# Performance work log

Measured on AMD Instinct MI355X. Metric: run time of the kernel, lower is better.

The kernel has to match this reference:

```python
import jax, jax.numpy as jnp
import numpy as np

N_AGENTS = 8
N_HEADS = 4
HYP = 128   # hypernet_embed
EMB = 32    # mixing_embed_dim


def _hypernet(entities, entity_mask, fc1_w, fc1_b, attn_w, out_w, out_b, fc2_w, fc2_b):
    # entities: [B, ne, ed]; entity_mask: [B, ne] (1 = masked/inactive)
    B, ne, _ = entities.shape
    hd = HYP // N_HEADS
    x1 = jax.nn.relu(entities @ fc1_w + fc1_b)                      # [B, ne, HYP]
    am = entity_mask[:, :N_AGENTS].astype(x1.dtype)                 # [B, na]
    em = entity_mask.astype(x1.dtype)                               # [B, ne]
    # attn_mask[b,i,j] = 1 - (1-am[i])*(1-em[j]): mask if agent i OR entity j inactive
    pre_mask = 1.0 - (1.0 - am)[:, :, None] * (1.0 - em)[:, None, :]  # [B, na, ne]
    # EntityAttentionLayer: agents are the queries, all entities are keys/values
    qkv = x1 @ attn_w                                               # [B, ne, 3*HYP] (no bias)
    q, k, v = jnp.split(qkv, 3, axis=-1)
    q = q[:, :N_AGENTS].reshape(B, N_AGENTS, N_HEADS, hd)
    k = k.reshape(B, ne, N_HEADS, hd)
    v = v.reshape(B, ne, N_HEADS, hd)
    scale = jnp.asarray(np.sqrt(hd), x1.dtype)
    logits = jnp.einsum('bqhd,bkhd->bhqk', q, k) / scale            # [B, H, na, ne]
    m = pre_mask[:, None, :, :]
    # masked softmax; fully-masked rows (torch: -inf -> NaN -> 0) become 0 via *(1-m)
    w = jax.nn.softmax(jnp.where(m > 0, -1e30, logits), axis=-1) * (1.0 - m)
    attn = jnp.einsum('bhqk,bkhd->bqhd', w, v).reshape(B, N_AGENTS, HYP)
    attn = attn @ out_w + out_b                                     # [B, na, HYP]
    keep = (1.0 - am)[:, :, None]                                   # zero masked agents (post_mask)
    attn = attn * keep
    x3 = (attn @ fc2_w + fc2_b) * keep                              # [B, na, EMB]
    return x3


def reference(agent_qs, entities, entity_mask, fc1_w, fc1_b, attn_w, out_w, out_b, fc2_w, fc2_b):
    bs, T, ne, ed = entities.shape
    B = bs * T
    ents = entities.reshape(B, ne, ed)
    emask = entity_mask.reshape(B, ne)
    qs = agent_qs.reshape(B, N_AGENTS)
    # 4 hypernets: 0=hyper_w_1 (matrix), 1=hyper_w_final (vector), 2=hyper_b_1 (vector), 3=V (scalar)
    outs = [_hypernet(ents, emask, fc1_w[i], fc1_b[i], attn_w[i], out_w[i],
                      out_b[i], fc2_w[i], fc2_b[i]) for i in range(4)]
    w1 = jax.nn.softmax(outs[0], axis=-1)                           # [B, na, EMB]
    b1 = outs[2].mean(axis=1)                                       # [B, EMB]
    hidden = jax.nn.elu(jnp.einsum('ba,bae->be', qs, w1) + b1)      # [B, EMB]
    w_final = jax.nn.softmax(outs[1].mean(axis=1), axis=-1)         # [B, EMB]
    v = outs[3].mean(axis=(1, 2))                                   # [B]
    y = jnp.sum(hidden * w_final, axis=-1) + v                      # [B]
    return y.reshape(bs, T, 1)


def setup_inputs() -> dict:
    key = jax.random.key(0)
    ks = jax.random.split(key, 10)
    bs, T, ne, ed = 128, 64, 16, 64
    s = 0.05
    return {
        'agent_qs': jax.random.normal(ks[0], (bs, T, N_AGENTS), jnp.float32),
        'entities': jax.random.normal(ks[1], (bs, T, ne, ed), jnp.float32),
        'entity_mask': jax.random.randint(ks[2], (bs, T, ne), 0, 2, jnp.int32),
        'fc1_w': jax.random.normal(ks[3], (4, ed, HYP), jnp.float32) * s,
        'fc1_b': jax.random.normal(ks[4], (4, HYP), jnp.float32) * s,
        'attn_w': jax.random.normal(ks[5], (4, HYP, 3 * HYP), jnp.float32) * s,
        'out_w': jax.random.normal(ks[6], (4, HYP, HYP), jnp.float32) * s,
        'out_b': jax.random.normal(ks[7], (4, HYP), jnp.float32) * s,
        'fc2_w': jax.random.normal(ks[8], (4, HYP, EMB), jnp.float32) * s,
        'fc2_b': jax.random.normal(ks[9], (4, EMB), jnp.float32) * s,
    }
```

## Files before the change

### kernel.cpp

```cpp
#include <hip/hip_runtime.h>
#include <math.h>

#define NAG 8
#define NE  16
#define ED  64
#define HYPD 128
#define QKVW 384
#define SB 2

#define X1S 132
#define KS  132
#define QS  132

#define OFF_X1    0
#define OFF_SLOG  0
#define OFF_ATTN  4224
#define OFF_K     8448
#define OFF_ATTN2 8448
#define OFF_Q     16896
#define OFF_OUT0  21120
#define OFF_MEANS 22144
#define OFF_EM    22912
#define LDS_BYTES 23040

typedef __attribute__((ext_vector_type(8))) short bf16x8;
typedef __attribute__((ext_vector_type(4))) short bf16x4;
typedef __attribute__((ext_vector_type(4))) float f32x4;

__device__ __forceinline__ short f2bf(float f) {
    union { float f; unsigned u; } c; c.f = f;
    unsigned r = (c.u + 0x7FFFu + ((c.u >> 16) & 1u)) >> 16;
    return (short)r;
}
__device__ __forceinline__ float bf2f(short s) {
    union { unsigned u; float f; } c; c.u = ((unsigned)(unsigned short)s) << 16; return c.f;
}
__device__ __forceinline__ bf16x8 ld_frag(const short* p) {
    bf16x4 lo = *(const bf16x4*)p;
    bf16x4 hi = *(const bf16x4*)(p + 16);
    return __builtin_shufflevector(lo, hi, 0, 1, 2, 3, 4, 5, 6, 7);
}

__global__ void pack_weights(const float* __restrict__ fc1_w,
                             const float* __restrict__ attn_w,
                             const float* __restrict__ out_w,
                             const float* __restrict__ fc2_w,
                             short* __restrict__ ws) {
    int gid = blockIdx.x * 256 + threadIdx.x;
    if (gid >= 608 * 64) return;
    int slot = gid >> 6, l = gid & 63;
    const float* src; int N, nt, kt;
    if (slot < 64) {
        int h = slot >> 4, f = slot & 15;
        nt = f >> 1; kt = f & 1; N = HYPD; src = fc1_w + h * ED * HYPD;
    } else if (slot < 448) {
        int s2 = slot - 64; int h = s2 / 96, f = s2 % 96;
        nt = f >> 2; kt = f & 3; N = QKVW; src = attn_w + h * HYPD * QKVW;
    } else if (slot < 576) {
        int s2 = slot - 448; int h = s2 >> 5, f = s2 & 31;
        nt = f >> 2; kt = f & 3; N = HYPD; src = out_w + h * HYPD * HYPD;
    } else {
        int s2 = slot - 576; int h = s2 >> 3, f = s2 & 7;
        nt = f >> 2; kt = f & 3; N = 32; src = fc2_w + h * HYPD * 32;
    }
    int rg = l >> 4, lc = l & 15;
    bf16x8 fr;
    #pragma unroll
    for (int j = 0; j < 8; ++j) {
        int k = kt * 32 + 4 * rg + (j & 3) + 16 * (j >> 2);
        fr[j] = f2bf(src[k * N + nt * 16 + lc]);
    }
    ((bf16x8*)ws)[slot * 64 + l] = fr;
}

__global__ __launch_bounds__(128, 2) void flexq_mfma(
    const float* __restrict__ agent_qs,
    const float* __restrict__ entities,
    const int*   __restrict__ entity_mask,
    const float* __restrict__ fc1_b,
    const float* __restrict__ out_b,
    const float* __restrict__ fc2_b,
    const short* __restrict__ wfrag,
    float* __restrict__ out, int B)
{
    __shared__ __align__(16) char smem[LDS_BYTES];
    short* x1    = (short*)(smem + OFF_X1);
    float* slog  = (float*)(smem + OFF_SLOG);
    short* attn  = (short*)(smem + OFF_ATTN);
    short* k     = (short*)(smem + OFF_K);
    short* attn2 = (short*)(smem + OFF_ATTN2);
    short* q     = (short*)(smem + OFF_Q);
    short* out0  = (short*)(smem + OFF_OUT0);
    float* means = (float*)(smem + OFF_MEANS);
    float* em    = (float*)(smem + OFF_EM);

    const int tid = threadIdx.x;
    const int l = tid & 63, w = tid >> 6;
    const int rg = l >> 4, lc = l & 15;
    const int b2 = blockIdx.x * SB;
    const bf16x8* WF = (const bf16x8*)wfrag;

    if (tid < 32)
        em[tid] = (entity_mask[(size_t)b2 * NE + tid] != 0) ? 1.0f : 0.0f;

    bf16x8 aent[2][2];
    #pragma unroll
    for (int kt = 0; kt < 2; ++kt)
        #pragma unroll
        for (int mt = 0; mt < 2; ++mt) {
            const float* ap = entities + ((size_t)(b2 + mt) * NE + lc) * ED + kt * 32 + rg * 4;
            float4 lo = *(const float4*)ap;
            float4 hi = *(const float4*)(ap + 16);
            bf16x8 af;
            af[0]=f2bf(lo.x); af[1]=f2bf(lo.y); af[2]=f2bf(lo.z); af[3]=f2bf(lo.w);
            af[4]=f2bf(hi.x); af[5]=f2bf(hi.y); af[6]=f2bf(hi.z); af[7]=f2bf(hi.w);
            aent[kt][mt] = af;
        }
    __syncthreads();

    for (int i = 0; i < 4; ++i) {
        {
            f32x4 acc[2][4];
            #pragma unroll
            for (int mt = 0; mt < 2; ++mt)
                #pragma unroll
                for (int n = 0; n < 4; ++n) acc[mt][n] = (f32x4){0.f,0.f,0.f,0.f};
            #pragma unroll
            for (int kt = 0; kt < 2; ++kt) {
                bf16x8 bn[4];
                #pragma unroll
                for (int n = 0; n < 4; ++n) bn[n] = WF[(i*16 + (4*w+n)*2 + kt)*64 + l];
                #pragma unroll
                for (int mt = 0; mt < 2; ++mt)
                    #pragma unroll
                    for (int n = 0; n < 4; ++n)
                        acc[mt][n] = __builtin_amdgcn_mfma_f32_16x16x32_bf16(aent[kt][mt], bn[n], acc[mt][n], 0,0,0);
            }
            #pragma unroll
            for (int n = 0; n < 4; ++n) {
                float bias = fc1_b[i*HYPD + (4*w+n)*16 + lc];
                #pragma unroll
                for (int mt = 0; mt < 2; ++mt)
                    #pragma unroll
                    for (int r = 0; r < 4; ++r)
                        x1[(16*mt + 4*rg + r)*X1S + (4*w+n)*16 + lc] = f2bf(fmaxf(acc[mt][n][r] + bias, 0.f));
            }
        }
        __syncthreads();

        f32x4 accv[2][4];
        {
            f32x4 acc[2][4];
            #pragma unroll
            for (int mt = 0; mt < 2; ++mt)
                #pragma unroll
                for (int j = 0; j < 4; ++j) acc[mt][j] = (f32x4){0.f,0.f,0.f,0.f};
            #pragma unroll
            for (int kt = 0; kt < 4; ++kt) {
                bf16x8 bj[4];
                #pragma unroll
                for (int j = 0; j < 4; ++j) bj[j] = WF[(64 + i*96 + (w + 2*j)*4 + kt)*64 + l];
                #pragma unroll
                for (int mt = 0; mt < 2; ++mt) {
                    bf16x8 a = ld_frag(x1 + (16*mt + lc)*X1S + kt*32 + rg*4);
                    #pragma unroll
                    for (int j = 0; j < 4; ++j)
                        acc[mt][j] = __builtin_amdgcn_mfma_f32_16x16x32_bf16(a, bj[j], acc[mt][j], 0,0,0);
                }
            }
            if (rg < 2) {
                #pragma unroll
                for (int j = 0; j < 4; ++j)
                    #pragma unroll
                    for (int mt = 0; mt < 2; ++mt)
                        #pragma unroll
                        for (int r = 0; r < 4; ++r)
                            q[(mt*NAG + 4*rg + r)*QS + (w + 2*j)*16 + lc] = f2bf(acc[mt][j][r]);
            }
        }
        {
            f32x4 acc[2][4];
            #pragma unroll
            for (int mt = 0; mt < 2; ++mt)
                #pragma unroll
                for (int j = 0; j < 4; ++j) acc[mt][j] = (f32x4){0.f,0.f,0.f,0.f};
            #pragma unroll
            for (int kt = 0; kt < 4; ++kt) {
                bf16x8 bj[4];
                #pragma unroll
                for (int j = 0; j < 4; ++j) bj[j] = WF[(64 + i*96 + (8 + w + 2*j)*4 + kt)*64 + l];
                #pragma unroll
                for (int mt = 0; mt < 2; ++mt) {
                    bf16x8 a = ld_frag(x1 + (16*mt + lc)*X1S + kt*32 + rg*4);
                    #pragma unroll
                    for (int j = 0; j < 4; ++j)
                        acc[mt][j] = __builtin_amdgcn_mfma_f32_16x16x32_bf16(a, bj[j], acc[mt][j], 0,0,0);
                }
            }
            #pragma unroll
            for (int j = 0; j < 4; ++j)
                #pragma unroll
                for (int mt = 0; mt < 2; ++mt)
                    #pragma unroll
                    for (int r = 0; r < 4; ++r)
                        k[(16*mt + 4*rg + r)*KS + (w + 2*j)*16 + lc] = f2bf(acc[mt][j][r]);
        }
        {
            #pragma unroll
            for (int mt = 0; mt < 2; ++mt)
                #pragma unroll
                for (int j = 0; j < 4; ++j) accv[mt][j] = (f32x4){0.f,0.f,0.f,0.f};
            #pragma unroll
            for (int kt = 0; kt < 4; ++kt) {
                bf16x8 bj[4];
                #pragma unroll
                for (int j = 0; j < 4; ++j) bj[j] = WF[(64 + i*96 + (16 + w + 2*j)*4 + kt)*64 + l];
                #pragma unroll
                for (int mt = 0; mt < 2; ++mt) {
                    bf16x8 a = ld_frag(x1 + (16*mt + lc)*X1S + kt*32 + rg*4);
                    #pragma unroll
                    for (int j = 0; j < 4; ++j)
                        accv[mt][j] = __builtin_amdgcn_mfma_f32_16x16x32_bf16(a, bj[j], accv[mt][j], 0,0,0);
                }
            }
        }
        __syncthreads();

        {
            #pragma unroll
            for (int h = 0; h < 4; ++h) {
                bf16x8 a  = ld_frag(q + (w*NAG + (lc & 7))*QS + h*32 + rg*4);
                bf16x8 bb = ld_frag(k + (w*NE  + lc)*KS       + h*32 + rg*4);
                f32x4 acc = (f32x4){0.f,0.f,0.f,0.f};
                acc = __builtin_amdgcn_mfma_f32_16x16x32_bf16(a, bb, acc, 0,0,0);
                if (rg < 2) {
                    #pragma unroll
                    for (int r = 0; r < 4; ++r)
                        slog[((w*4 + h)*NAG + 4*rg + r)*16 + lc] = acc[r] * 0.17677669529663687f;
                }
            }
        }
        __syncthreads();

        if (tid < 64) {
            int s = tid >> 5, h = (tid >> 3) & 3, qi = tid & 7;
            float am = em[s*NE + qi];
            float* rowp = slog + ((s*4 + h)*NAG + qi)*16;
            float mx = -3.0e38f; bool any = false;
            #pragma unroll
            for (int kk = 0; kk < NE; ++kk)
                if (em[s*NE + kk] == 0.f) { any = true; mx = fmaxf(mx, rowp[kk]); }
            if (am != 0.f || !any) {
                #pragma unroll
                for (int kk = 0; kk < NE; ++kk) rowp[kk] = 0.f;
            } else {
                float eb[NE]; float sum = 0.f;
                #pragma unroll
                for (int kk = 0; kk < NE; ++kk) {
                    float e = (em[s*NE + kk] == 0.f) ? __expf(rowp[kk] - mx) : 0.f;
                    eb[kk] = e; sum += e;
                }
                float inv = 1.f / sum;
                #pragma unroll
                for (int kk = 0; kk < NE; ++kk) rowp[kk] = eb[kk] * inv;
            }
        }
        __syncthreads();

        {
            #pragma unroll
            for (int vt = 0; vt < 4; ++vt) {
                int c = w + 2*vt;
                int h = c >> 1;
                #pragma unroll
                for (int mt = 0; mt < 2; ++mt) {
                    f32x4 pw = *(const f32x4*)(slog + ((mt*4 + h)*NAG + (lc & 7))*16 + 4*rg);
                    bf16x8 a;
                    a[0]=f2bf(pw[0]); a[1]=f2bf(pw[1]); a[2]=f2bf(pw[2]); a[3]=f2bf(pw[3]);
                    a[4]=0; a[5]=0; a[6]=0; a[7]=0;
                    bf16x8 bb;
                    bb[0]=f2bf(accv[mt][vt][0]); bb[1]=f2bf(accv[mt][vt][1]);
                    bb[2]=f2bf(accv[mt][vt][2]); bb[3]=f2bf(accv[mt][vt][3]);
                    bb[4]=0; bb[5]=0; bb[6]=0; bb[7]=0;
                    f32x4 po = (f32x4){0.f,0.f,0.f,0.f};
                    po = __builtin_amdgcn_mfma_f32_16x16x32_bf16(a, bb, po, 0,0,0);
                    if (rg < 2) {
                        #pragma unroll
                        for (int r = 0; r < 4; ++r)
                            attn[(mt*NAG + 4*rg + r)*X1S + c*16 + lc] = f2bf(po[r]);
                    }
                }
            }
        }
        __syncthreads();

        {
            f32x4 acc[4];
            #pragma unroll
            for (int n = 0; n < 4; ++n) acc[n] = (f32x4){0.f,0.f,0.f,0.f};
            #pragma unroll
            for (int kt = 0; kt < 4; ++kt) {
                bf16x8 bn[4];
                #pragma unroll
                for (int n = 0; n < 4; ++n) bn[n] = WF[(448 + i*32 + (4*w+n)*4 + kt)*64 + l];
                bf16x8 a = ld_frag(attn + lc*X1S + kt*32 + rg*4);
                #pragma unroll
                for (int n = 0; n < 4; ++n)
                    acc[n] = __builtin_amdgcn_mfma_f32_16x16x32_bf16(a, bn[n], acc[n], 0,0,0);
            }
            #pragma unroll
            for (int n = 0; n < 4; ++n) {
                float bias = out_b[i*HYPD + (4*w+n)*16 + lc];
                #pragma unroll
                for (int r = 0; r < 4; ++r) {
                    int row = 4*rg + r;
                    float keep = 1.f - em[(row >> 3)*NE + (row & 7)];
                    attn2[row*X1S + (4*w+n)*16 + lc] = f2bf((acc[n][r] + bias) * keep);
                }
            }
        }
        __syncthreads();

        {
            f32x4 acc = (f32x4){0.f,0.f,0.f,0.f};
            #pragma unroll
            for (int kt = 0; kt < 4; ++kt) {
                bf16x8 a = ld_frag(attn2 + lc*X1S + kt*32 + rg*4);
                bf16x8 bfr = WF[(576 + i*8 + w*4 + kt)*64 + l];
                acc = __builtin_amdgcn_mfma_f32_16x16x32_bf16(a, bfr, acc, 0,0,0);
            }
            float bias = fc2_b[i*32 + w*16 + lc];
            float vals[4];
            #pragma unroll
            for (int r = 0; r < 4; ++r) {
                int row = 4*rg + r;
                float keep = 1.f - em[(row >> 3)*NE + (row & 7)];
                vals[r] = (acc[r] + bias) * keep;
            }
            if (i == 0) {
                #pragma unroll
                for (int r = 0; r < 4; ++r)
                    out0[(4*rg + r)*32 + w*16 + lc] = f2bf(vals[r]);
            } else {
                float ps = vals[0] + vals[1] + vals[2] + vals[3];
                ps += __shfl_xor(ps, 16);
                if ((rg & 1) == 0) {
                    int s = rg >> 1;
                    means[(i-1)*64 + s*32 + w*16 + lc] = ps;
                }
            }
        }
        __syncthreads();
    }

    if (l < 32) {
        int s = w, c = l;
        float s1 = means[0*64 + s*32 + c] * 0.125f;
        float b1 = means[1*64 + s*32 + c] * 0.125f;
        float vsum = means[2*64 + s*32 + c];

        float hid = 0.f;
        #pragma unroll
        for (int a = 0; a < NAG; ++a) {
            float x = bf2f(out0[(s*NAG + a)*32 + c]);
            float mx = x;
            #pragma unroll
            for (int m = 16; m >= 1; m >>= 1) mx = fmaxf(mx, __shfl_xor(mx, m, 32));
            float e = __expf(x - mx);
            float sum = e;
            #pragma unroll
            for (int m = 16; m >= 1; m >>= 1) sum += __shfl_xor(sum, m, 32);
            float qsv = agent_qs[(size_t)(b2 + s)*NAG + a];
            hid += qsv * (e / sum);
        }
        hid += b1;
        hid = (hid > 0.f) ? hid : expm1f(hid);

        float mx = s1;
        #pragma unroll
        for (int m = 16; m >= 1; m >>= 1) mx = fmaxf(mx, __shfl_xor(mx, m, 32));
        float e = __expf(s1 - mx);
        float ss = e;
        #pragma unroll
        for (int m = 16; m >= 1; m >>= 1) ss += __shfl_xor(ss, m, 32);
        float wf = e / ss;

        float red = hid * wf + vsum * (1.f / 256.f);
        #pragma unroll
        for (int m = 16; m >= 1; m >>= 1) red += __shfl_xor(red, m, 32);
        if (c == 0) out[b2 + s] = red;
    }
}

#define QKVP 388
#define NTHR 384
__device__ __forceinline__ float4 f4load(const float* p) { return *reinterpret_cast<const float4*>(p); }
__device__ __forceinline__ void f4store(float* p, const float4& v) { *reinterpret_cast<float4*>(p) = v; }
__device__ __forceinline__ void f4fma(float4& a, float s, const float4& w) {
    a.x += s * w.x; a.y += s * w.y; a.z += s * w.z; a.w += s * w.w;
}

__global__ __launch_bounds__(NTHR) void flexq_fp32(
    const float* __restrict__ agent_qs, const float* __restrict__ entities,
    const int* __restrict__ entity_mask, const float* __restrict__ fc1_w,
    const float* __restrict__ fc1_b, const float* __restrict__ attn_w,
    const float* __restrict__ out_w, const float* __restrict__ out_b,
    const float* __restrict__ fc2_w, const float* __restrict__ fc2_b,
    float* __restrict__ out)
{
    const int b = blockIdx.x, tid = threadIdx.x;
    __shared__ float s_ent[NE][ED];
    __shared__ float s_x1t[HYPD][NE];
    __shared__ float s_qkv[NE][QKVP];
    __shared__ float s_w[4][NAG][NE];
    __shared__ float s_attn[NAG][HYPD];
    __shared__ float s_attnout[NAG][HYPD];
    __shared__ float s_outs[4][NAG][32];
    __shared__ float s_mask[NE];
    __shared__ float s_qs[NAG];

    const float* ent = entities + (size_t)b * NE * ED;
    for (int o = tid; o < NE * ED; o += NTHR) s_ent[o >> 6][o & 63] = ent[o];
    if (tid < NE) s_mask[tid] = (entity_mask[(size_t)b * NE + tid] != 0) ? 1.0f : 0.0f;
    if (tid < NAG) s_qs[tid] = agent_qs[(size_t)b * NAG + tid];
    __syncthreads();

    for (int i = 0; i < 4; ++i) {
        {
            const float* W1 = fc1_w + i * ED * HYPD;
            const float* B1 = fc1_b + i * HYPD;
            for (int o4 = tid; o4 < 512; o4 += NTHR) {
                int e = o4 >> 5, j = (o4 & 31) * 4;
                float4 acc = f4load(B1 + j);
                for (int d = 0; d < ED; ++d) { float x = s_ent[e][d]; f4fma(acc, x, f4load(W1 + d * HYPD + j)); }
                s_x1t[j+0][e] = fmaxf(acc.x, 0.f); s_x1t[j+1][e] = fmaxf(acc.y, 0.f);
                s_x1t[j+2][e] = fmaxf(acc.z, 0.f); s_x1t[j+3][e] = fmaxf(acc.w, 0.f);
            }
        }
        __syncthreads();
        {
            const float* W2 = attn_w + i * HYPD * QKVW;
            int j = (tid % 96) * 4, e0 = (tid / 96) * 4;
            float4 a0 = {0,0,0,0}, a1 = {0,0,0,0}, a2 = {0,0,0,0}, a3 = {0,0,0,0};
            for (int d = 0; d < HYPD; ++d) {
                float4 wv = f4load(W2 + d * QKVW + j);
                float4 x = f4load(&s_x1t[d][e0]);
                f4fma(a0, x.x, wv); f4fma(a1, x.y, wv); f4fma(a2, x.z, wv); f4fma(a3, x.w, wv);
            }
            f4store(&s_qkv[e0+0][j], a0); f4store(&s_qkv[e0+1][j], a1);
            f4store(&s_qkv[e0+2][j], a2); f4store(&s_qkv[e0+3][j], a3);
        }
        __syncthreads();
        {
            const float inv_scale = 0.17677669529663687f;
            for (int o = tid; o < 512; o += NTHR) {
                int h = o >> 7, qi = (o >> 4) & 7, kk = o & 15;
                const float* qp = &s_qkv[qi][h * 32];
                const float* kp = &s_qkv[kk][HYPD + h * 32];
                float s = 0.f;
                #pragma unroll
                for (int d4 = 0; d4 < 8; ++d4) {
                    float4 qv = f4load(qp + 4 * d4), kv2 = f4load(kp + 4 * d4);
                    s += qv.x*kv2.x + qv.y*kv2.y + qv.z*kv2.z + qv.w*kv2.w;
                }
                s_w[h][qi][kk] = s * inv_scale;
            }
        }
        __syncthreads();
        if (tid < 32) {
            int h = tid >> 3, qi = tid & 7;
            float am = s_mask[qi];
            float mx = -3.0e38f; bool any = false;
            #pragma unroll
            for (int kk = 0; kk < NE; ++kk)
                if (s_mask[kk] == 0.f) { any = true; mx = fmaxf(mx, s_w[h][qi][kk]); }
            if (am != 0.f || !any) {
                #pragma unroll
                for (int kk = 0; kk < NE; ++kk) s_w[h][qi][kk] = 0.f;
            } else {
                float eb[NE]; float sum = 0.f;
                #pragma unroll
                for (int kk = 0; kk < NE; ++kk) {
                    float e = (s_mask[kk] == 0.f) ? __expf(s_w[h][qi][kk] - mx) : 0.f;
                    eb[kk] = e; sum += e;
                }
                float inv = 1.f / sum;
                #pragma unroll
                for (int kk = 0; kk < NE; ++kk) s_w[h][qi][kk] = eb[kk] * inv;
            }
        }
        __syncthreads();
        if (tid < 256) {
            int qi = tid >> 5, j = (tid & 31) * 4, h = j >> 5, d0 = j & 31;
            float4 acc = {0,0,0,0};
            #pragma unroll
            for (int kk = 0; kk < NE; ++kk) f4fma(acc, s_w[h][qi][kk], f4load(&s_qkv[kk][2*HYPD + h*32 + d0]));
            f4store(&s_attn[qi][j], acc);
        }
        __syncthreads();
        if (tid < 256) {
            const float* W3 = out_w + i * HYPD * HYPD;
            const float* B3 = out_b + i * HYPD;
            int qi = tid >> 5, j = (tid & 31) * 4;
            float4 acc = f4load(B3 + j);
            for (int d = 0; d < HYPD; ++d) f4fma(acc, s_attn[qi][d], f4load(W3 + d * HYPD + j));
            float keep = 1.f - s_mask[qi];
            acc.x *= keep; acc.y *= keep; acc.z *= keep; acc.w *= keep;
            f4store(&s_attnout[qi][j], acc);
        }
        __syncthreads();
        if (tid < 64) {
            const float* W4 = fc2_w + i * HYPD * 32;
            const float* B4 = fc2_b + i * 32;
            int qi = tid >> 3, c = (tid & 7) * 4;
            float4 acc = f4load(B4 + c);
            for (int d = 0; d < HYPD; ++d) f4fma(acc, s_attnout[qi][d], f4load(W4 + d * 32 + c));
            float keep = 1.f - s_mask[qi];
            acc.x *= keep; acc.y *= keep; acc.z *= keep; acc.w *= keep;
            f4store(&s_outs[i][qi][c], acc);
        }
        __syncthreads();
    }

    if (tid < 32) {
        const int c = tid;
        float b1 = 0.f, s1 = 0.f, vs = 0.f;
        #pragma unroll
        for (int qi = 0; qi < NAG; ++qi) {
            b1 += s_outs[2][qi][c]; s1 += s_outs[1][qi][c]; vs += s_outs[3][qi][c];
        }
        b1 *= 0.125f; s1 *= 0.125f;
        float hid = 0.f;
        #pragma unroll
        for (int a = 0; a < NAG; ++a) {
            float x = s_outs[0][a][c];
            float mx = x;
            #pragma unroll
            for (int m = 16; m >= 1; m >>= 1) mx = fmaxf(mx, __shfl_xor(mx, m, 32));
            float e = __expf(x - mx);
            float sm = e;
            #pragma unroll
            for (int m = 16; m >= 1; m >>= 1) sm += __shfl_xor(sm, m, 32);
            hid += s_qs[a] * (e / sm);
        }
        hid += b1;
        hid = (hid > 0.f) ? hid : expm1f(hid);
        float mx = s1;
        #pragma unroll
        for (int m = 16; m >= 1; m >>= 1) mx = fmaxf(mx, __shfl_xor(mx, m, 32));
        float e = __expf(s1 - mx);
        float ssum = e;
        #pragma unroll
        for (int m = 16; m >= 1; m >>= 1) ssum += __shfl_xor(ssum, m, 32);
        float wf = e / ssum;
        float red = hid * wf + vs * (1.f / 256.f);
        #pragma unroll
        for (int m = 16; m >= 1; m >>= 1) red += __shfl_xor(red, m, 32);
        if (tid == 0) out[b] = red;
    }
}

extern "C" void kernel_launch(void* const* d_in, const int* in_sizes, int n_in,
                              void* d_out, int out_size, void* d_ws, size_t ws_size,
                              hipStream_t stream) {
    const float* agent_qs    = (const float*)d_in[0];
    const float* entities    = (const float*)d_in[1];
    const int*   entity_mask = (const int*)  d_in[2];
    const float* fc1_w       = (const float*)d_in[3];
    const float* fc1_b       = (const float*)d_in[4];
    const float* attn_w      = (const float*)d_in[5];
    const float* out_w       = (const float*)d_in[6];
    const float* out_b       = (const float*)d_in[7];
    const float* fc2_w       = (const float*)d_in[8];
    const float* fc2_b       = (const float*)d_in[9];
    float* out = (float*)d_out;

    const int B = in_sizes[0] / NAG;

    if (ws_size >= (size_t)(608 * 1024) && (B % SB) == 0) {
        pack_weights<<<152, 256, 0, stream>>>(fc1_w, attn_w, out_w, fc2_w, (short*)d_ws);
        flexq_mfma<<<B / SB, 128, 0, stream>>>(agent_qs, entities, entity_mask,
                                               fc1_b, out_b, fc2_b,
                                               (const short*)d_ws, out, B);
    } else {
        flexq_fp32<<<B, NTHR, 0, stream>>>(agent_qs, entities, entity_mask,
                                           fc1_w, fc1_b, attn_w, out_w, out_b,
                                           fc2_w, fc2_b, out);
    }
}
```

Baseline: 199.0 us.

## Give each wave its own sample and LDS arena to drop block barriers

Restructures the MFMA kernel so each wavefront processes one sample independently in a private LDS arena, with four waves per 256-thread block. Before, two waves cooperated on two samples and split the N dimension, which needed many __syncthreads between stages. Now all block barriers are removed and each wave computes every N tile of its own sample. The cost is that weight fragments are no longer shared across the M dimension within a wave, so each wave reloads the full weight set per sample. LDS per block grows, and register pressure rises with 8 accumulators per stage.

```diff
diff --git a/kernel.cpp b/kernel.cpp
--- a/kernel.cpp
+++ b/kernel.cpp
@@ -6,22 +6,14 @@
 #define ED  64
 #define HYPD 128
 #define QKVW 384
-#define SB 2
+#define SB 4
 
 #define X1S 132
 #define KS  132
 #define QS  132
 
-#define OFF_X1    0
-#define OFF_SLOG  0
-#define OFF_ATTN  4224
-#define OFF_K     8448
-#define OFF_ATTN2 8448
-#define OFF_Q     16896
-#define OFF_OUT0  21120
-#define OFF_MEANS 22144
-#define OFF_EM    22912
-#define LDS_BYTES 23040
+#define WARENA 11520
+#define LDS_BYTES (4 * WARENA)
 
 typedef __attribute__((ext_vector_type(8))) short bf16x8;
 typedef __attribute__((ext_vector_type(4))) short bf16x4;
@@ -73,7 +65,7 @@
     ((bf16x8*)ws)[slot * 64 + l] = fr;
 }
 
-__global__ __launch_bounds__(128, 2) void flexq_mfma(
+__global__ __launch_bounds__(256, 2) void flexq_mfma(
     const float* __restrict__ agent_qs,
     const float* __restrict__ entities,
     const int*   __restrict__ entity_mask,
@@ -84,172 +76,137 @@
     float* __restrict__ out, int B)
 {
     __shared__ __align__(16) char smem[LDS_BYTES];
-    short* x1    = (short*)(smem + OFF_X1);
-    float* slog  = (float*)(smem + OFF_SLOG);
-    short* attn  = (short*)(smem + OFF_ATTN);
-    short* k     = (short*)(smem + OFF_K);
-    short* attn2 = (short*)(smem + OFF_ATTN2);
-    short* q     = (short*)(smem + OFF_Q);
-    short* out0  = (short*)(smem + OFF_OUT0);
-    float* means = (float*)(smem + OFF_MEANS);
-    float* em    = (float*)(smem + OFF_EM);
-
     const int tid = threadIdx.x;
     const int l = tid & 63, w = tid >> 6;
     const int rg = l >> 4, lc = l & 15;
-    const int b2 = blockIdx.x * SB;
+    const int ss = blockIdx.x * SB + w;
     const bf16x8* WF = (const bf16x8*)wfrag;
 
-    if (tid < 32)
-        em[tid] = (entity_mask[(size_t)b2 * NE + tid] != 0) ? 1.0f : 0.0f;
-
-    bf16x8 aent[2][2];
+    char* ws0 = smem + w * WARENA;
+    short* x1    = (short*)(ws0);
+    float* slog  = (float*)(ws0);
+    short* attn  = (short*)(ws0 + 2112);
+    short* k     = (short*)(ws0 + 4224);
+    short* attn2 = (short*)(ws0 + 4224);
+    short* q     = (short*)(ws0 + 8448);
+    short* out0  = (short*)(ws0 + 10560);
+    float* means = (float*)(ws0 + 11072);
+    float* em    = (float*)(ws0 + 11456);
+
+    if (l < 16)
+        em[l] = (entity_mask[(size_t)ss * NE + l] != 0) ? 1.0f : 0.0f;
+
+    bf16x8 aent[2];
     #pragma unroll
-    for (int kt = 0; kt < 2; ++kt)
-        #pragma unroll
-        for (int mt = 0; mt < 2; ++mt) {
-            const float* ap = entities + ((size_t)(b2 + mt) * NE + lc) * ED + kt * 32 + rg * 4;
-            float4 lo = *(const float4*)ap;
-            float4 hi = *(const float4*)(ap + 16);
-            bf16x8 af;
-            af[0]=f2bf(lo.x); af[1]=f2bf(lo.y); af[2]=f2bf(lo.z); af[3]=f2bf(lo.w);
-            af[4]=f2bf(hi.x); af[5]=f2bf(hi.y); af[6]=f2bf(hi.z); af[7]=f2bf(hi.w);
-            aent[kt][mt] = af;
-        }
-    __syncthreads();
+    for (int kt = 0; kt < 2; ++kt) {
+        const float* ap = entities + ((size_t)ss * NE + lc) * ED + kt * 32 + rg * 4;
+        float4 lo = *(const float4*)ap;
+        float4 hi = *(const float4*)(ap + 16);
+        bf16x8 af;
+        af[0]=f2bf(lo.x); af[1]=f2bf(lo.y); af[2]=f2bf(lo.z); af[3]=f2bf(lo.w);
+        af[4]=f2bf(hi.x); af[5]=f2bf(hi.y); af[6]=f2bf(hi.z); af[7]=f2bf(hi.w);
+        aent[kt] = af;
+    }
 
     for (int i = 0; i < 4; ++i) {
         {
-            f32x4 acc[2][4];
-            #pragma unroll
-            for (int mt = 0; mt < 2; ++mt)
-                #pragma unroll
-                for (int n = 0; n < 4; ++n) acc[mt][n] = (f32x4){0.f,0.f,0.f,0.f};
-            #pragma unroll
-            for (int kt = 0; kt < 2; ++kt) {
-                bf16x8 bn[4];
-                #pragma unroll
-                for (int n = 0; n < 4; ++n) bn[n] = WF[(i*16 + (4*w+n)*2 + kt)*64 + l];
-                #pragma unroll
-                for (int mt = 0; mt < 2; ++mt)
-                    #pragma unroll
-                    for (int n = 0; n < 4; ++n)
-                        acc[mt][n] = __builtin_amdgcn_mfma_f32_16x16x32_bf16(aent[kt][mt], bn[n], acc[mt][n], 0,0,0);
-            }
-            #pragma unroll
-            for (int n = 0; n < 4; ++n) {
-                float bias = fc1_b[i*HYPD + (4*w+n)*16 + lc];
-                #pragma unroll
-                for (int mt = 0; mt < 2; ++mt)
+            f32x4 acc[8];
+            #pragma unroll
+            for (int n = 0; n < 8; ++n) acc[n] = (f32x4){0.f,0.f,0.f,0.f};
+            #pragma unroll
+            for (int kt = 0; kt < 2; ++kt)
+                #pragma unroll
+                for (int n = 0; n < 8; ++n) {
+                    bf16x8 bn = WF[(i*16 + n*2 + kt)*64 + l];
+                    acc[n] = __builtin_amdgcn_mfma_f32_16x16x32_bf16(aent[kt], bn, acc[n], 0,0,0);
+                }
+            #pragma unroll
+            for (int n = 0; n < 8; ++n) {
+                float bias = fc1_b[i*HYPD + n*16 + lc];
+                #pragma unroll
+                for (int r = 0; r < 4; ++r)
+                    x1[(4*rg + r)*X1S + n*16 + lc] = f2bf(fmaxf(acc[n][r] + bias, 0.f));
+            }
+        }
+
+        f32x4 accv[8];
+        {
+            f32x4 acc[8];
+            #pragma unroll
+            for (int n = 0; n < 8; ++n) acc[n] = (f32x4){0.f,0.f,0.f,0.f};
+            #pragma unroll
+            for (int kt = 0; kt < 4; ++kt) {
+                bf16x8 a = ld_frag(x1 + lc*X1S + kt*32 + rg*4);
+                #pragma unroll
+                for (int n = 0; n < 8; ++n) {
+                    bf16x8 bn = WF[(64 + i*96 + n*4 + kt)*64 + l];
+                    acc[n] = __builtin_amdgcn_mfma_f32_16x16x32_bf16(a, bn, acc[n], 0,0,0);
+                }
+            }
+            if (rg < 2) {
+                #pragma unroll
+                for (int n = 0; n < 8; ++n)
                     #pragma unroll
                     for (int r = 0; r < 4; ++r)
-                        x1[(16*mt + 4*rg + r)*X1S + (4*w+n)*16 + lc] = f2bf(fmaxf(acc[mt][n][r] + bias, 0.f));
-            }
-        }
-        __syncthreads();
-
-        f32x4 accv[2][4];
-        {
-            f32x4 acc[2][4];
-            #pragma unroll
-            for (int mt = 0; mt < 2; ++mt)
-                #pragma unroll
-                for (int j = 0; j < 4; ++j) acc[mt][j] = (f32x4){0.f,0.f,0.f,0.f};
+                        q[(4*rg + r)*QS + n*16 + lc] = f2bf(acc[n][r]);
+            }
+        }
+        {
+            f32x4 acc[8];
+            #pragma unroll
+            for (int n = 0; n < 8; ++n) acc[n] = (f32x4){0.f,0.f,0.f,0.f};
             #pragma unroll
             for (int kt = 0; kt < 4; ++kt) {
-                bf16x8 bj[4];
-                #pragma unroll
-                for (int j = 0; j < 4; ++j) bj[j] = WF[(64 + i*96 + (w + 2*j)*4 + kt)*64 + l];
-                #pragma unroll
-                for (int mt = 0; mt < 2; ++mt) {
-                    bf16x8 a = ld_frag(x1 + (16*mt + lc)*X1S + kt*32 + rg*4);
-                    #pragma unroll
-                    for (int j = 0; j < 4; ++j)
-                        acc[mt][j] = __builtin_amdgcn_mfma_f32_16x16x32_bf16(a, bj[j], acc[mt][j], 0,0,0);
-                }
-            }
-            if (rg < 2) {
-                #pragma unroll
-                for (int j = 0; j < 4; ++j)
-                    #pragma unroll
-                    for (int mt = 0; mt < 2; ++mt)
-                        #pragma unroll
-                        for (int r = 0; r < 4; ++r)
-                            q[(mt*NAG + 4*rg + r)*QS + (w + 2*j)*16 + lc] = f2bf(acc[mt][j][r]);
-            }
-        }
-        {
-            f32x4 acc[2][4];
-            #pragma unroll
-            for (int mt = 0; mt < 2; ++mt)
-                #pragma unroll
-                for (int j = 0; j < 4; ++j) acc[mt][j] = (f32x4){0.f,0.f,0.f,0.f};
+                bf16x8 a = ld_frag(x1 + lc*X1S + kt*32 + rg*4);
+                #pragma unroll
+                for (int n = 0; n < 8; ++n) {
+                    bf16x8 bn = WF[(64 + i*96 + (8 + n)*4 + kt)*64 + l];
+                    acc[n] = __builtin_amdgcn_mfma_f32_16x16x32_bf16(a, bn, acc[n], 0,0,0);
+                }
+            }
+            #pragma unroll
+            for (int n = 0; n < 8; ++n)
+                #pragma unroll
+                for (int r = 0; r < 4; ++r)
+                    k[(4*rg + r)*KS + n*16 + lc] = f2bf(acc[n][r]);
+        }
+        {
+            #pragma unroll
+            for (int n = 0; n < 8; ++n) accv[n] = (f32x4){0.f,0.f,0.f,0.f};
             #pragma unroll
             for (int kt = 0; kt < 4; ++kt) {
-                bf16x8 bj[4];
-                #pragma unroll
-                for (int j = 0; j < 4; ++j) bj[j] = WF[(64 + i*96 + (8 + w + 2*j)*4 + kt)*64 + l];
-                #pragma unroll
-                for (int mt = 0; mt < 2; ++mt) {
-                    bf16x8 a = ld_frag(x1 + (16*mt + lc)*X1S + kt*32 + rg*4);
-                    #pragma unroll
-                    for (int j = 0; j < 4; ++j)
-                        acc[mt][j] = __builtin_amdgcn_mfma_f32_16x16x32_bf16(a, bj[j], acc[mt][j], 0,0,0);
-                }
-            }
-            #pragma unroll
-            for (int j = 0; j < 4; ++j)
-                #pragma unroll
-                for (int mt = 0; mt < 2; ++mt)
-                    #pragma unroll
-                    for (int r = 0; r < 4; ++r)
-                        k[(16*mt + 4*rg + r)*KS + (w + 2*j)*16 + lc] = f2bf(acc[mt][j][r]);
-        }
-        {
-            #pragma unroll
-            for (int mt = 0; mt < 2; ++mt)
-                #pragma unroll
-                for (int j = 0; j < 4; ++j) accv[mt][j] = (f32x4){0.f,0.f,0.f,0.f};
-            #pragma unroll
-            for (int kt = 0; kt < 4; ++kt) {
-                bf16x8 bj[4];
-                #pragma unroll
-                for (int j = 0; j < 4; ++j) bj[j] = WF[(64 + i*96 + (16 + w + 2*j)*4 + kt)*64 + l];
-                #pragma unroll
-                for (int mt = 0; mt < 2; ++mt) {
-                    bf16x8 a = ld_frag(x1 + (16*mt + lc)*X1S + kt*32 + rg*4);
-                    #pragma unroll
-                    for (int j = 0; j < 4; ++j)
-                        accv[mt][j] = __builtin_amdgcn_mfma_f32_16x16x32_bf16(a, bj[j], accv[mt][j], 0,0,0);
-                }
-            }
-        }
-        __syncthreads();
+                bf16x8 a = ld_frag(x1 + lc*X1S + kt*32 + rg*4);
+                #pragma unroll
+                for (int n = 0; n < 8; ++n) {
+                    bf16x8 bn = WF[(64 + i*96 + (16 + n)*4 + kt)*64 + l];
+                    accv[n] = __builtin_amdgcn_mfma_f32_16x16x32_bf16(a, bn, accv[n], 0,0,0);
+                }
+            }
+        }
 
         {
             #pragma unroll
             for (int h = 0; h < 4; ++h) {
-                bf16x8 a  = ld_frag(q + (w*NAG + (lc & 7))*QS + h*32 + rg*4);
-                bf16x8 bb = ld_frag(k + (w*NE  + lc)*KS       + h*32 + rg*4);
+                bf16x8 a  = ld_frag(q + (lc & 7)*QS + h*32 + rg*4);
+                bf16x8 bb = ld_frag(k + lc*KS       + h*32 + rg*4);
                 f32x4 acc = (f32x4){0.f,0.f,0.f,0.f};
                 acc = __builtin_amdgcn_mfma_f32_16x16x32_bf16(a, bb, acc, 0,0,0);
                 if (rg < 2) {
                     #pragma unroll
                     for (int r = 0; r < 4; ++r)
-                        slog[((w*4 + h)*NAG + 4*rg + r)*16 + lc] = acc[r] * 0.17677669529663687f;
-                }
-            }
-        }
-        __syncthreads();
-
-        if (tid < 64) {
-            int s = tid >> 5, h = (tid >> 3) & 3, qi = tid & 7;
-            float am = em[s*NE + qi];
-            float* rowp = slog + ((s*4 + h)*NAG + qi)*16;
+                        slog[(h*NAG + 4*rg + r)*16 + lc] = acc[r] * 0.17677669529663687f;
+                }
+            }
+        }
+
+        if (l < 32) {
+            int qi = l & 7;
+            float am = em[qi];
+            float* rowp = slog + l*16;
             float mx = -3.0e38f; bool any = false;
             #pragma unroll
             for (int kk = 0; kk < NE; ++kk)
-                if (em[s*NE + kk] == 0.f) { any = true; mx = fmaxf(mx, rowp[kk]); }
+                if (em[kk] == 0.f) { any = true; mx = fmaxf(mx, rowp[kk]); }
             if (am != 0.f || !any) {
                 #pragma unroll
                 for (int kk = 0; kk < NE; ++kk) rowp[kk] = 0.f;
@@ -257,7 +214,7 @@
                 float eb[NE]; float sum = 0.f;
                 #pragma unroll
                 for (int kk = 0; kk < NE; ++kk) {
-                    float e = (em[s*NE + kk] == 0.f) ? __expf(rowp[kk] - mx) : 0.f;
+                    float e = (em[kk] == 0.f) ? __expf(rowp[kk] - mx) : 0.f;
                     eb[kk] = e; sum += e;
                 }
                 float inv = 1.f / sum;
@@ -265,104 +222,104 @@
                 for (int kk = 0; kk < NE; ++kk) rowp[kk] = eb[kk] * inv;
             }
         }
-        __syncthreads();
-
-        {
-            #pragma unroll
-            for (int vt = 0; vt < 4; ++vt) {
-                int c = w + 2*vt;
+
+        {
+            #pragma unroll
+            for (int c = 0; c < 8; ++c) {
                 int h = c >> 1;
-                #pragma unroll
-                for (int mt = 0; mt < 2; ++mt) {
-                    f32x4 pw = *(const f32x4*)(slog + ((mt*4 + h)*NAG + (lc & 7))*16 + 4*rg);
-                    bf16x8 a;
-                    a[0]=f2bf(pw[0]); a[1]=f2bf(pw[1]); a[2]=f2bf(pw[2]); a[3]=f2bf(pw[3]);
-                    a[4]=0; a[5]=0; a[6]=0; a[7]=0;
-                    bf16x8 bb;
-                    bb[0]=f2bf(accv[mt][vt][0]); bb[1]=f2bf(accv[mt][vt][1]);
-                    bb[2]=f2bf(accv[mt][vt][2]); bb[3]=f2bf(accv[mt][vt][3]);
-                    bb[4]=0; bb[5]=0; bb[6]=0; bb[7]=0;
-                    f32x4 po = (f32x4){0.f,0.f,0.f,0.f};
-                    po = __builtin_amdgcn_mfma_f32_16x16x32_bf16(a, bb, po, 0,0,0);
-                    if (rg < 2) {
+                f32x4 pw = *(const f32x4*)(slog + (h*NAG + (lc & 7))*16 + 4*rg);
+                bf16x8 a;
+                a[0]=f2bf(pw[0]); a[1]=f2bf(pw[1]); a[2]=f2bf(pw[2]); a[3]=f2bf(pw[3]);
+                a[4]=0; a[5]=0; a[6]=0; a[7]=0;
+                bf16x8 bb;
+                bb[0]=f2bf(accv[c][0]); bb[1]=f2bf(accv[c][1]);
+                bb[2]=f2bf(accv[c][2]); bb[3]=f2bf(accv[c][3]);
+                bb[4]=0; bb[5]=0; bb[6]=0; bb[7]=0;
+                f32x4 po = (f32x4){0.f,0.f,0.f,0.f};
+                po = __builtin_amdgcn_mfma_f32_16x16x32_bf16(a, bb, po, 0,0,0);
+                if (rg < 2) {
+                    #pragma unroll
+                    for (int r = 0; r < 4; ++r)
+                        attn[(4*rg + r)*X1S + c*16 + lc] = f2bf(po[r]);
+                }
+            }
+        }
+
+        {
+            f32x4 acc[8];
+            #pragma unroll
+            for (int n = 0; n < 8; ++n) acc[n] = (f32x4){0.f,0.f,0.f,0.f};
+            #pragma unroll
+            for (int kt = 0; kt < 4; ++kt) {
+                bf16x8 a = ld_frag(attn + lc*X1S + kt*32 + rg*4);
+                #pragma unroll
+                for (int n = 0; n < 8; ++n) {
+                    bf16x8 bn = WF[(448 + i*32 + n*4 + kt)*64 + l];
+                    acc[n] = __builtin_amdgcn_mfma_f32_16x16x32_bf16(a, bn, acc[n], 0,0,0);
+                }
+            }
+            if (rg < 2) {
+                #pragma unroll
+                for (int n = 0; n < 8; ++n) {
+                    float bias = out_b[i*HYPD + n*16 + lc];
+                    #pragma unroll
+                    for (int r = 0; r < 4; ++r) {
+                        int row = 4*rg + r;
+                        float keep = 1.f - em[row];
+                        attn2[row*X1S + n*16 + lc] = f2bf((acc[n][r] + bias) * keep);
+                    }
+                }
+            }
+        }
+
+        {
+            f32x4 acc[2];
+            acc[0] = (f32x4){0.f,0.f,0.f,0.f};
+            acc[1] = (f32x4){0.f,0.f,0.f,0.f};
+            #pragma unroll
+            for (int kt = 0; kt < 4; ++kt) {
+                bf16x8 a = ld_frag(attn2 + lc*X1S + kt*32 + rg*4);
+                #pragma unroll
+                for (int n = 0; n < 2; ++n) {
+                    bf16x8 bn = WF[(576 + i*8 + n*4 + kt)*64 + l];
+                    acc[n] = __builtin_amdgcn_mfma_f32_16x16x32_bf16(a, bn, acc[n], 0,0,0);
+                }
+            }
+            #pragma unroll
+            for (int n = 0; n < 2; ++n) {
+                float bias = fc2_b[i*32 + n*16 + lc];
+                float vals[4];
+                #pragma unroll
+                for (int r = 0; r < 4; ++r) {
+                    int row = 4*rg + r;
+                    float keep = (row < 8) ? (1.f - em[row]) : 0.f;
+                    vals[r] = (acc[n][r] + bias) * keep;
+                }
+                if (i == 0) {
+                    if (rg < 2)
                         #pragma unroll
                         for (int r = 0; r < 4; ++r)
-                            attn[(mt*NAG + 4*rg + r)*X1S + c*16 + lc] = f2bf(po[r]);
-                    }
-                }
-            }
-        }
-        __syncthreads();
-
-        {
-            f32x4 acc[4];
-            #pragma unroll
-            for (int n = 0; n < 4; ++n) acc[n] = (f32x4){0.f,0.f,0.f,0.f};
-            #pragma unroll
-            for (int kt = 0; kt < 4; ++kt) {
-                bf16x8 bn[4];
-                #pragma unroll
-                for (int n = 0; n < 4; ++n) bn[n] = WF[(448 + i*32 + (4*w+n)*4 + kt)*64 + l];
-                bf16x8 a = ld_frag(attn + lc*X1S + kt*32 + rg*4);
-                #pragma unroll
-                for (int n = 0; n < 4; ++n)
-                    acc[n] = __builtin_amdgcn_mfma_f32_16x16x32_bf16(a, bn[n], acc[n], 0,0,0);
-            }
-            #pragma unroll
-            for (int n = 0; n < 4; ++n) {
-                float bias = out_b[i*HYPD + (4*w+n)*16 + lc];
-                #pragma unroll
-                for (int r = 0; r < 4; ++r) {
-                    int row = 4*rg + r;
-                    float keep = 1.f - em[(row >> 3)*NE + (row & 7)];
-                    attn2[row*X1S + (4*w+n)*16 + lc] = f2bf((acc[n][r] + bias) * keep);
-                }
-            }
-        }
-        __syncthreads();
-
-        {
-            f32x4 acc = (f32x4){0.f,0.f,0.f,0.f};
-            #pragma unroll
-            for (int kt = 0; kt < 4; ++kt) {
-                bf16x8 a = ld_frag(attn2 + lc*X1S + kt*32 + rg*4);
-                bf16x8 bfr = WF[(576 + i*8 + w*4 + kt)*64 + l];
-                acc = __builtin_amdgcn_mfma_f32_16x16x32_bf16(a, bfr, acc, 0,0,0);
-            }
-            float bias = fc2_b[i*32 + w*16 + lc];
-            float vals[4];
-            #pragma unroll
-            for (int r = 0; r < 4; ++r) {
-                int row = 4*rg + r;
-                float keep = 1.f - em[(row >> 3)*NE + (row & 7)];
-                vals[r] = (acc[r] + bias) * keep;
-            }
-            if (i == 0) {
-                #pragma unroll
-                for (int r = 0; r < 4; ++r)
-                    out0[(4*rg + r)*32 + w*16 + lc] = f2bf(vals[r]);
-            } else {
-                float ps = vals[0] + vals[1] + vals[2] + vals[3];
-                ps += __shfl_xor(ps, 16);
-                if ((rg & 1) == 0) {
-                    int s = rg >> 1;
-                    means[(i-1)*64 + s*32 + w*16 + lc] = ps;
-                }
-            }
-        }
-        __syncthreads();
+                            out0[(4*rg + r)*32 + n*16 + lc] = f2bf(vals[r]);
+                } else {
+                    float ps = vals[0] + vals[1] + vals[2] + vals[3];
+                    ps += __shfl_xor(ps, 16);
+                    if (rg == 0)
+                        means[(i-1)*32 + n*16 + lc] = ps;
+                }
+            }
+        }
     }
 
     if (l < 32) {
-        int s = w, c = l;
-        float s1 = means[0*64 + s*32 + c] * 0.125f;
-        float b1 = means[1*64 + s*32 + c] * 0.125f;
-        float vsum = means[2*64 + s*32 + c];
+        int c = l;
+        float s1 = means[0*32 + c] * 0.125f;
+        float b1 = means[1*32 + c] * 0.125f;
+        float vsum = means[2*32 + c];
 
         float hid = 0.f;
         #pragma unroll
         for (int a = 0; a < NAG; ++a) {
-            float x = bf2f(out0[(s*NAG + a)*32 + c]);
+            float x = bf2f(out0[a*32 + c]);
             float mx = x;
             #pragma unroll
             for (int m = 16; m >= 1; m >>= 1) mx = fmaxf(mx, __shfl_xor(mx, m, 32));
@@ -370,7 +327,7 @@
             float sum = e;
             #pragma unroll
             for (int m = 16; m >= 1; m >>= 1) sum += __shfl_xor(sum, m, 32);
-            float qsv = agent_qs[(size_t)(b2 + s)*NAG + a];
+            float qsv = agent_qs[(size_t)ss*NAG + a];
             hid += qsv * (e / sum);
         }
         hid += b1;
@@ -380,15 +337,15 @@
         #pragma unroll
         for (int m = 16; m >= 1; m >>= 1) mx = fmaxf(mx, __shfl_xor(mx, m, 32));
         float e = __expf(s1 - mx);
-        float ss = e;
-        #pragma unroll
-        for (int m = 16; m >= 1; m >>= 1) ss += __shfl_xor(ss, m, 32);
-        float wf = e / ss;
+        float ssm = e;
+        #pragma unroll
+        for (int m = 16; m >= 1; m >>= 1) ssm += __shfl_xor(ssm, m, 32);
+        float wf = e / ssm;
 
         float red = hid * wf + vsum * (1.f / 256.f);
         #pragma unroll
         for (int m = 16; m >= 1; m >>= 1) red += __shfl_xor(red, m, 32);
-        if (c == 0) out[b2 + s] = red;
+        if (c == 0) out[ss] = red;
     }
 }
 
@@ -579,7 +536,7 @@
 
     if (ws_size >= (size_t)(608 * 1024) && (B % SB) == 0) {
         pack_weights<<<152, 256, 0, stream>>>(fc1_w, attn_w, out_w, fc2_w, (short*)d_ws);
-        flexq_mfma<<<B / SB, 128, 0, stream>>>(agent_qs, entities, entity_mask,
+        flexq_mfma<<<B / SB, 256, 0, stream>>>(agent_qs, entities, entity_mask,
                                                fc1_b, out_b, fc2_b,
                                                (const short*)d_ws, out, B);
     } else {
```

After: 192.8 us. 3.1% less time.
